# Performance work log

Measured on AMD Instinct MI355X. Metric: run time of the kernel, lower is better.

The kernel has to match this reference:

```python
import jax, jax.numpy as jnp
import numpy as np

N = 50000        # num nodes
E = 1_000_000    # num edges
F_IN = 256       # input feature dim
UNITS = 128      # hidden units
NUM_CLASSES = 40 # output classes
EPS = 1e-3       # Keras BatchNormalization default epsilon


def setup_inputs() -> dict:
    key = jax.random.key(0)
    ks = jax.random.split(key, 32)
    inp = {
        "x": jax.random.normal(ks[0], (N, F_IN), jnp.float32),
        "edge_index": jax.random.randint(ks[1], (2, E), 0, N, jnp.int32),
        "edge_weight": jax.random.uniform(ks[2], (E,), jnp.float32),
    }
    dims = [(F_IN, UNITS), (UNITS, UNITS), (UNITS, NUM_CLASSES)]
    ki = 3
    for li, (fi, fo) in enumerate(dims, 1):
        inp[f"w_gcn{li}"] = jax.random.normal(ks[ki], (fi, fo), jnp.float32) / np.sqrt(fi).astype(np.float32); ki += 1
        inp[f"w_self{li}"] = jax.random.normal(ks[ki], (fi, fo), jnp.float32) / np.sqrt(fi).astype(np.float32); ki += 1
        inp[f"b{li}"] = jnp.zeros((fo,), jnp.float32)
        inp[f"gamma{li}"] = 1.0 + 0.1 * jax.random.normal(ks[ki], (fo,), jnp.float32); ki += 1
        inp[f"beta{li}"] = 0.1 * jax.random.normal(ks[ki], (fo,), jnp.float32); ki += 1
        inp[f"mean{li}"] = 0.1 * jax.random.normal(ks[ki], (fo,), jnp.float32); ki += 1
        inp[f"var{li}"] = jnp.ones((fo,), jnp.float32)
    return inp


def _gcn_bs(h, src, dst, norm_w, w_gcn, w_self, b, gamma, beta, mean, var, act):
    # GCN aggregation: transform then gather->weight->scatter-sum
    hw = h @ w_gcn                                   # [N, out]
    msg = hw[src] * norm_w[:, None]                  # [E, out]
    agg = jax.ops.segment_sum(msg, dst, num_segments=N)
    out = agg + h @ w_self + b                       # self-loop dense + bias
    # BatchNorm (inference: moving stats)
    out = (out - mean) * jax.lax.rsqrt(var + EPS) * gamma + beta
    return act(out) if act is not None else out


def reference(x, edge_index, edge_weight,
              w_gcn1, w_self1, b1, gamma1, beta1, mean1, var1,
              w_gcn2, w_self2, b2, gamma2, beta2, mean2, var2,
              w_gcn3, w_self3, b3, gamma3, beta3, mean3, var3):
    src, dst = edge_index[0], edge_index[1]
    # symmetric GCN normalization (renorm=False: no added self loops)
    deg = jax.ops.segment_sum(edge_weight, dst, num_segments=N)
    dinv = jnp.where(deg > 0, jax.lax.rsqrt(jnp.where(deg > 0, deg, 1.0)), 0.0)
    norm_w = dinv[src] * edge_weight * dinv[dst]
    # inference: DropEdge and Dropout are identity
    h = _gcn_bs(x, src, dst, norm_w, w_gcn1, w_self1, b1, gamma1, beta1, mean1, var1, jax.nn.relu)
    h = _gcn_bs(h, src, dst, norm_w, w_gcn2, w_self2, b2, gamma2, beta2, mean2, var2, jax.nn.relu)
    h = _gcn_bs(h, src, dst, norm_w, w_gcn3, w_self3, b3, gamma3, beta3, mean3, var3, None)
    return h
```

## Files before the change

kernel.cpp:

```cpp
#include <hip/hip_runtime.h>
#include <hip/hip_bf16.h>

#define NN 50000
#define EE 1000000
static constexpr float EPSV = 1e-3f;
static constexpr float FIXSCALE = 16777216.f;

typedef __attribute__((ext_vector_type(8))) short short8;
typedef __attribute__((ext_vector_type(4))) float fx4;

__device__ inline float blo(unsigned u) { return __uint_as_float(u << 16); }
__device__ inline float bhi(unsigned u) { return __uint_as_float(u & 0xffff0000u); }
__device__ inline unsigned short f2b(float f) {
    __hip_bfloat16 h = __float2bfloat16(f);
    return *(unsigned short*)&h;
}
__device__ inline unsigned pack2(float a, float b) {
    return (unsigned)f2b(a) | ((unsigned)f2b(b) << 16);
}

__device__ inline void gload_lds16(const unsigned short* g, unsigned short* ldsbase) {
    __builtin_amdgcn_global_load_lds(
        (const __attribute__((address_space(1))) unsigned int*)(const void*)g,
        (__attribute__((address_space(3))) unsigned int*)(void*)ldsbase, 16, 0, 0);
}


#define ZB 391
#define WB1 256
#define WB2 128
#define WB3 64

__global__ void setup_kernel(float* __restrict__ zp,
                             const float* __restrict__ wg1, const float* __restrict__ ws1,
                             unsigned short* __restrict__ Wt1,
                             const float* __restrict__ wg2, const float* __restrict__ ws2,
                             unsigned short* __restrict__ Wt2,
                             const float* __restrict__ wg3, const float* __restrict__ ws3,
                             unsigned short* __restrict__ Wt3) {
    int b = blockIdx.x;
    int t = threadIdx.x;
    if (b < ZB) {
        int i = b * 256 + t;
        if (i < 100096) zp[i] = 0.f;
    } else if (b < ZB + WB1) {
        int idx = (b - ZB) * 256 + t;
        int n = idx >> 8, k = idx & 255;
        float v = (n < 128) ? wg1[(size_t)k * 128 + n]
                            : ws1[(size_t)k * 128 + (n - 128)];
        Wt1[idx] = f2b(v);
    } else if (b < ZB + WB1 + WB2) {
        int idx = (b - ZB - WB1) * 256 + t;
        int n = idx >> 7, k = idx & 127;
        float v = (n < 128) ? wg2[(size_t)k * 128 + n]
                            : ws2[(size_t)k * 128 + (n - 128)];
        Wt2[idx] = f2b(v);
    } else {
        int idx = (b - ZB - WB1 - WB2) * 256 + t;
        int n = idx >> 7, k = idx & 127;
        float v = 0.f;
        if (n < 40) v = wg3[(size_t)k * 40 + n];
        else if (n < 80) v = ws3[(size_t)k * 40 + (n - 40)];
        Wt3[idx] = f2b(v);
    }
}


template <bool AF32>
__device__ __forceinline__ void gemm_body(int bx, int by, const void* __restrict__ Av,
                                          const unsigned short* __restrict__ Wt,
                                          const float* __restrict__ bias,
                                          unsigned short* __restrict__ Cg,
                                          unsigned short* __restrict__ Cs,
                                          int M, int K, int Fo,
                                          unsigned short* sA, unsigned short* sB) {
    const int t = threadIdx.x;
    const int lane = t & 63;
    const int wave = t >> 6;
    const int wm = wave >> 1, wn = wave & 1;
    const int l15 = lane & 15, quad = lane >> 4;
    const int row0 = bx * 128;
    const int colbase = by * 128;

    fx4 acc[4][4];
#pragma unroll
    for (int r = 0; r < 4; ++r)
#pragma unroll
        for (int c = 0; c < 4; ++c) acc[r][c] = (fx4){0.f, 0.f, 0.f, 0.f};

    for (int kc = 0; kc < K; kc += 64) {
#pragma unroll
        for (int j = 0; j < 4; ++j) {
            int c = wave * 4 + j;
            int rb = c >> 1, kh = c & 1;
            int ar = row0 + rb * 16 + l15;
            if (ar >= M) ar = M - 1;
            int ak = kc + kh * 32 + quad * 8;
            if constexpr (AF32) {
                const float* Af = (const float*)Av;
                const float4* p = (const float4*)(Af + (size_t)ar * K + ak);
                float4 v0 = p[0], v1 = p[1];
                uint4 u;
                u.x = pack2(v0.x, v0.y);
                u.y = pack2(v0.z, v0.w);
                u.z = pack2(v1.x, v1.y);
                u.w = pack2(v1.z, v1.w);
                *reinterpret_cast<uint4*>(sA + c * 512 + lane * 8) = u;
            } else {
                gload_lds16((const unsigned short*)Av + (size_t)ar * K + ak, sA + c * 512);
            }
            int br = colbase + rb * 16 + l15;
            gload_lds16(Wt + (size_t)br * K + ak, sB + c * 512);
        }
        __syncthreads();

#pragma unroll
        for (int kh = 0; kh < 2; ++kh) {
            short8 a[4], b[4];
#pragma unroll
            for (int r = 0; r < 4; ++r)
                a[r] = *reinterpret_cast<const short8*>(&sA[((wm * 4 + r) * 2 + kh) * 512 + lane * 8]);
#pragma unroll
            for (int c = 0; c < 4; ++c)
                b[c] = *reinterpret_cast<const short8*>(&sB[((wn * 4 + c) * 2 + kh) * 512 + lane * 8]);
#pragma unroll
            for (int r = 0; r < 4; ++r)
#pragma unroll
                for (int c = 0; c < 4; ++c)
                    acc[r][c] = __builtin_amdgcn_mfma_f32_16x16x32_bf16(a[r], b[c], acc[r][c], 0, 0, 0);
        }
        __syncthreads();
    }

#pragma unroll
    for (int c = 0; c < 4; ++c) {
        int f = colbase + wn * 64 + c * 16 + l15;
        if (f >= 2 * Fo) continue;
        bool isG = (f < Fo);
        int col = isG ? f : f - Fo;
        float badd = isG ? 0.f : bias[col];
        unsigned short* base = isG ? Cg : Cs;
#pragma unroll
        for (int r = 0; r < 4; ++r) {
#pragma unroll
            for (int reg = 0; reg < 4; ++reg) {
                int row = row0 + wm * 64 + r * 16 + quad * 4 + reg;
                if (row < M) base[(size_t)row * Fo + col] = f2b(acc[r][c][reg] + badd);
            }
        }
    }
}


#define CB 3907
#define GX1 391

__global__ __launch_bounds__(256) void pre2_kernel(
    const int* __restrict__ ei, const float* __restrict__ ew,
    unsigned long long* __restrict__ cnt64, unsigned* __restrict__ rank,
    const float* __restrict__ x, const unsigned short* __restrict__ Wt1,
    const float* __restrict__ bias1,
    unsigned short* __restrict__ Cg, unsigned short* __restrict__ Cs) {
    __shared__ unsigned short sA[128 * 64];
    __shared__ unsigned short sB[128 * 64];
    int b = blockIdx.x;
    if (b < CB) {
        int e = b * 256 + threadIdx.x;
        if (e < EE) {
            int d = ei[EE + e];
            unsigned fx = __float2uint_rn(ew[e] * FIXSCALE);
            unsigned long long old =
                atomicAdd(&cnt64[d], 0x100000000ull | (unsigned long long)fx);
            rank[e] = (unsigned)(old >> 32);
        }
        return;
    }
    int gi = b - CB;
    int by = gi / GX1;
    int bx = gi - by * GX1;
    gemm_body<true>(bx, by, x, Wt1, bias1, Cg, Cs, NN, 256, 128, sA, sB);
}

template <bool AF32>
__global__ __launch_bounds__(256) void gemm_mfma(const void* __restrict__ Ab,
                                                 const unsigned short* __restrict__ Wt,
                                                 const float* __restrict__ bias,
                                                 unsigned short* __restrict__ Cg,
                                                 unsigned short* __restrict__ Cs,
                                                 int M, int K, int Fo) {
    __shared__ unsigned short sA[128 * 64];
    __shared__ unsigned short sB[128 * 64];
    gemm_body<AF32>(blockIdx.x, blockIdx.y, Ab, Wt, bias, Cg, Cs, M, K, Fo, sA, sB);
}


__global__ __launch_bounds__(1024) void dinvsum_kernel(const uint2* __restrict__ cnt64,
                                                       float* __restrict__ dinv,
                                                       int* __restrict__ bsum) {
    __shared__ int s[1024];
    const int t = threadIdx.x;
    int idx = blockIdx.x * 1024 + t;
    uint2 cv = make_uint2(0u, 0u);
    if (idx < NN) cv = cnt64[idx];
    float deg = (float)cv.x * (1.f / FIXSCALE);
    if (idx < NN) dinv[idx] = (deg > 0.f) ? rsqrtf(deg) : 0.f;
    s[t] = (int)cv.y;
    __syncthreads();
#pragma unroll
    for (int off = 512; off > 0; off >>= 1) {
        if (t < off) s[t] += s[t + off];
        __syncthreads();
    }
    if (t == 0) bsum[blockIdx.x] = s[0];
}

__global__ __launch_bounds__(64) void scanB_kernel(const int* __restrict__ bsum,
                                                   int* __restrict__ bpre, int nb) {
    int t = threadIdx.x;
    int v = (t < nb) ? bsum[t] : 0;
    int own = v;
#pragma unroll
    for (int off = 1; off < 64; off <<= 1) {
        int u = __shfl_up(v, off);
        if (t >= off) v += u;
    }
    if (t < nb) bpre[t] = v - own;
}

__global__ __launch_bounds__(1024) void scanC_kernel(const uint2* __restrict__ cnt64,
                                                     const int* __restrict__ bpre,
                                                     int* __restrict__ rowstart) {
    __shared__ int s[1024];
    const int t = threadIdx.x;
    int idx = blockIdx.x * 1024 + t;
    int v = (idx < NN) ? (int)cnt64[idx].y : 0;
    s[t] = v;
    __syncthreads();
#pragma unroll
    for (int off = 1; off < 1024; off <<= 1) {
        int u = (t >= off) ? s[t - off] : 0;
        __syncthreads();
        s[t] += u;
        __syncthreads();
    }
    if (idx < NN) rowstart[idx] = s[t] - v + bpre[blockIdx.x];
    if (idx == 0) rowstart[NN] = EE;
}

__global__ void fill_kernel(const int* __restrict__ ei, const float* __restrict__ ew,
                            const float* __restrict__ dinv, const int* __restrict__ rowstart,
                            const unsigned* __restrict__ rank, unsigned* __restrict__ eprec4) {
    int e = blockIdx.x * blockDim.x + threadIdx.x;
    if (e >= EE) return;
    int s = ei[e], d = ei[EE + e];
    int idx = rowstart[d] + (int)rank[e];
    float w = dinv[s] * ew[e] * dinv[d];
    eprec4[idx] = ((unsigned)s << 16) | (unsigned)f2b(w);
}


template <bool RELU>
__global__ __launch_bounds__(256) void agg128_kernel(
    const int* __restrict__ rowstart, const unsigned* __restrict__ eprec4,
    const unsigned* __restrict__ hw, const unsigned* __restrict__ selfC,
    const float* __restrict__ g, const float* __restrict__ be,
    const float* __restrict__ mu, const float* __restrict__ va,
    unsigned* __restrict__ out) {
    int wave = threadIdx.x >> 6;
    int lane = threadIdx.x & 63;
    int n = blockIdx.x * 4 + wave;
    if (n >= NN) return;
    unsigned scp = selfC[n * 64 + lane];
    float acc0 = blo(scp), acc1 = bhi(scp);
    int beg = rowstart[n], end = rowstart[n + 1];
    int i = beg;
    for (; i + 4 <= end; i += 4) {
        unsigned e0 = eprec4[i], e1 = eprec4[i + 1], e2 = eprec4[i + 2], e3 = eprec4[i + 3];
        unsigned v0 = hw[(e0 >> 16) * 64u + lane];
        unsigned v1 = hw[(e1 >> 16) * 64u + lane];
        unsigned v2 = hw[(e2 >> 16) * 64u + lane];
        unsigned v3 = hw[(e3 >> 16) * 64u + lane];
        float w0 = blo(e0), w1 = blo(e1), w2 = blo(e2), w3 = blo(e3);
        acc0 += blo(v0) * w0; acc1 += bhi(v0) * w0;
        acc0 += blo(v1) * w1; acc1 += bhi(v1) * w1;
        acc0 += blo(v2) * w2; acc1 += bhi(v2) * w2;
        acc0 += blo(v3) * w3; acc1 += bhi(v3) * w3;
    }
    for (; i < end; ++i) {
        unsigned e = eprec4[i];
        unsigned v = hw[(e >> 16) * 64u + lane];
        float w = blo(e);
        acc0 += blo(v) * w; acc1 += bhi(v) * w;
    }
    float2 m2 = reinterpret_cast<const float2*>(mu)[lane];
    float2 v2f = reinterpret_cast<const float2*>(va)[lane];
    float2 g2 = reinterpret_cast<const float2*>(g)[lane];
    float2 b2 = reinterpret_cast<const float2*>(be)[lane];
    float r0 = (acc0 - m2.x) * rsqrtf(v2f.x + EPSV) * g2.x + b2.x;
    float r1 = (acc1 - m2.y) * rsqrtf(v2f.y + EPSV) * g2.y + b2.y;
    if (RELU) {
        r0 = fmaxf(r0, 0.f);
        r1 = fmaxf(r1, 0.f);
    }
    out[n * 64 + lane] = pack2(r0, r1);
}


__global__ __launch_bounds__(256) void agg40_kernel(
    const int* __restrict__ rowstart, const unsigned* __restrict__ eprec4,
    const unsigned* __restrict__ hw, const unsigned* __restrict__ selfC,
    const float* __restrict__ g, const float* __restrict__ be,
    const float* __restrict__ mu, const float* __restrict__ va,
    float* __restrict__ out) {
    int wave = threadIdx.x >> 6;
    int lane = threadIdx.x & 63;
    int n = blockIdx.x * 4 + wave;
    if (n >= NN) return;
    int grp = lane / 20;
    int fl = lane - grp * 20;
    float acc0 = 0.f, acc1 = 0.f;
    int beg = rowstart[n], end = rowstart[n + 1];
    if (grp < 3) {
        for (int i = beg + grp; i < end; i += 3) {
            unsigned e = eprec4[i];
            unsigned v = hw[(e >> 16) * 20u + fl];
            float w = blo(e);
            acc0 += blo(v) * w;
            acc1 += bhi(v) * w;
        }
    }
    acc0 += __shfl(acc0, lane + 20) + __shfl(acc0, lane + 40);
    acc1 += __shfl(acc1, lane + 20) + __shfl(acc1, lane + 40);
    if (lane < 20) {
        int f0 = lane * 2;
        unsigned scp = selfC[n * 20 + lane];
        acc0 += blo(scp);
        acc1 += bhi(scp);
        float2 m2 = reinterpret_cast<const float2*>(mu)[lane];
        float2 v2f = reinterpret_cast<const float2*>(va)[lane];
        float2 g2 = reinterpret_cast<const float2*>(g)[lane];
        float2 b2 = reinterpret_cast<const float2*>(be)[lane];
        float r0 = (acc0 - m2.x) * rsqrtf(v2f.x + EPSV) * g2.x + b2.x;
        float r1 = (acc1 - m2.y) * rsqrtf(v2f.y + EPSV) * g2.y + b2.y;
        *reinterpret_cast<float2*>(&out[(size_t)n * 40 + f0]) = make_float2(r0, r1);
    }
}


extern "C" void kernel_launch(void* const* d_in, const int* in_sizes, int n_in,
                              void* d_out, int out_size, void* d_ws, size_t ws_size,
                              hipStream_t stream) {
    const float* x = (const float*)d_in[0];
    const int* ei = (const int*)d_in[1];
    const float* ew = (const float*)d_in[2];

    const float* wg[3]  = {(const float*)d_in[3],  (const float*)d_in[10], (const float*)d_in[17]};
    const float* wsf[3] = {(const float*)d_in[4],  (const float*)d_in[11], (const float*)d_in[18]};
    const float* bs[3]  = {(const float*)d_in[5],  (const float*)d_in[12], (const float*)d_in[19]};
    const float* gm[3]  = {(const float*)d_in[6],  (const float*)d_in[13], (const float*)d_in[20]};
    const float* bt[3]  = {(const float*)d_in[7],  (const float*)d_in[14], (const float*)d_in[21]};
    const float* mu[3]  = {(const float*)d_in[8],  (const float*)d_in[15], (const float*)d_in[22]};
    const float* vr[3]  = {(const float*)d_in[9],  (const float*)d_in[16], (const float*)d_in[23]};

    float* W = (float*)d_ws;
    unsigned long long* cnt64 = (unsigned long long*)W;
    float* dinv     = W + 100096;
    unsigned* rank  = (unsigned*)(W + 150144);
    int*   bsum     = (int*)(W + 1150144);
    int*   bpre     = (int*)(W + 1150208);
    int*   rowstart = (int*)(W + 1150272);
    unsigned* eprec4 = (unsigned*)(W + 1200384);
    unsigned short* Wt1 = (unsigned short*)(W + 2200384);
    unsigned short* Wt2 = (unsigned short*)(W + 2233152);
    unsigned short* Wt3 = (unsigned short*)(W + 2249536);
    unsigned short* bufH = (unsigned short*)(W + 2257728);
    unsigned short* bufHW = (unsigned short*)(W + 8657728);
    unsigned short* bufSb = (unsigned short*)(W + 11857728);

    const int B = 256;
    const int SB = 49;

    setup_kernel<<<ZB + WB1 + WB2 + WB3, B, 0, stream>>>(
        W, wg[0], wsf[0], Wt1, wg[1], wsf[1], Wt2, wg[2], wsf[2], Wt3);

    pre2_kernel<<<CB + 2 * GX1, B, 0, stream>>>(
        ei, ew, cnt64, rank, x, Wt1, bs[0], bufHW, bufSb);

    dinvsum_kernel<<<SB, 1024, 0, stream>>>((const uint2*)cnt64, dinv, bsum);
    scanB_kernel<<<1, 64, 0, stream>>>(bsum, bpre, SB);
    scanC_kernel<<<SB, 1024, 0, stream>>>((const uint2*)cnt64, bpre, rowstart);
    fill_kernel<<<(EE + B - 1) / B, B, 0, stream>>>(ei, ew, dinv, rowstart, rank, eprec4);

    const int aggGrid = (NN + 3) / 4;
    dim3 g2((NN + 127) / 128, 2), g1((NN + 127) / 128, 1);

    agg128_kernel<true><<<aggGrid, B, 0, stream>>>(rowstart, eprec4, (const unsigned*)bufHW,
                                                   (const unsigned*)bufSb, gm[0], bt[0], mu[0], vr[0],
                                                   (unsigned*)bufH);

    gemm_mfma<false><<<g2, B, 0, stream>>>(bufH, Wt2, bs[1], bufHW, bufSb, NN, 128, 128);
    agg128_kernel<true><<<aggGrid, B, 0, stream>>>(rowstart, eprec4, (const unsigned*)bufHW,
                                                   (const unsigned*)bufSb, gm[1], bt[1], mu[1], vr[1],
                                                   (unsigned*)bufH);

    gemm_mfma<false><<<g1, B, 0, stream>>>(bufH, Wt3, bs[2], bufHW, bufSb, NN, 128, 40);
    agg40_kernel<<<aggGrid, B, 0, stream>>>(rowstart, eprec4, (const unsigned*)bufHW,
                                            (const unsigned*)bufSb, gm[2], bt[2], mu[2], vr[2],
                                            (float*)d_out);
}
```

Before: 415.1 us.

## Specialize layer-1 GEMM with smaller tiles and batch degree-count atomics per thread

The fused pre-pass kernel gets a dedicated layer-1 GEMM that uses 64x128 tiles with a 32-wide K step and smaller LDS buffers, doubling the number of GEMM blocks. The degree-counting blocks now handle four edges per thread, issuing all loads before the atomics, so there are four times fewer counting blocks. The aim is better occupancy and load balance between the atomic work and the GEMM work in the shared launch, plus more memory-level parallelism in the counting phase. The trade-off is less A/B reuse per tile and more K-loop barriers in layer 1.

After: 424.1 us. +2.2%, slower.

```diff
diff --git a/kernel.cpp b/kernel.cpp
--- a/kernel.cpp
+++ b/kernel.cpp
@@ -66,21 +66,142 @@
 }
 
 
-template <bool AF32>
-__device__ __forceinline__ void gemm_body(int bx, int by, const void* __restrict__ Av,
-                                          const unsigned short* __restrict__ Wt,
-                                          const float* __restrict__ bias,
-                                          unsigned short* __restrict__ Cg,
-                                          unsigned short* __restrict__ Cs,
-                                          int M, int K, int Fo,
-                                          unsigned short* sA, unsigned short* sB) {
+#define CB4 977
+#define GX1 782
+#define GB1 1564
+
+__device__ __forceinline__ void gemm1_body(int bx, int by, const float* __restrict__ x,
+                                           const unsigned short* __restrict__ Wt,
+                                           const float* __restrict__ bias,
+                                           unsigned short* __restrict__ Cg,
+                                           unsigned short* __restrict__ Cs,
+                                           unsigned short* sA, unsigned short* sB) {
+    const int t = threadIdx.x;
+    const int lane = t & 63;
+    const int wave = t >> 6;
+    const int l15 = lane & 15, quad = lane >> 4;
+    const int row0 = bx * 64;
+    const int colbase = by * 128;
+
+    fx4 acc[4][2];
+#pragma unroll
+    for (int r = 0; r < 4; ++r)
+#pragma unroll
+        for (int c = 0; c < 2; ++c) acc[r][c] = (fx4){0.f, 0.f, 0.f, 0.f};
+
+    for (int kc = 0; kc < 256; kc += 32) {
+#pragma unroll
+        for (int j = 0; j < 3; ++j) {
+            int op = wave * 3 + j;
+            int ak = kc + quad * 8;
+            if (op < 4) {
+                int ar = row0 + op * 16 + l15;
+                if (ar >= NN) ar = NN - 1;
+                const float4* p = (const float4*)(x + (size_t)ar * 256 + ak);
+                float4 v0 = p[0], v1 = p[1];
+                uint4 u;
+                u.x = pack2(v0.x, v0.y);
+                u.y = pack2(v0.z, v0.w);
+                u.z = pack2(v1.x, v1.y);
+                u.w = pack2(v1.z, v1.w);
+                *reinterpret_cast<uint4*>(sA + op * 512 + lane * 8) = u;
+            } else {
+                int bi = op - 4;
+                int br = colbase + bi * 16 + l15;
+                gload_lds16(Wt + (size_t)br * 256 + ak, sB + bi * 512);
+            }
+        }
+        __syncthreads();
+
+        short8 a[4], bf[2];
+#pragma unroll
+        for (int r = 0; r < 4; ++r)
+            a[r] = *reinterpret_cast<const short8*>(&sA[r * 512 + lane * 8]);
+#pragma unroll
+        for (int c = 0; c < 2; ++c)
+            bf[c] = *reinterpret_cast<const short8*>(&sB[(wave * 2 + c) * 512 + lane * 8]);
+#pragma unroll
+        for (int r = 0; r < 4; ++r)
+#pragma unroll
+            for (int c = 0; c < 2; ++c)
+                acc[r][c] = __builtin_amdgcn_mfma_f32_16x16x32_bf16(a[r], bf[c], acc[r][c], 0, 0, 0);
+        __syncthreads();
+    }
+
+#pragma unroll
+    for (int c = 0; c < 2; ++c) {
+        int f = colbase + wave * 32 + c * 16 + l15;
+        bool isG = (f < 128);
+        int col = isG ? f : f - 128;
+        float badd = isG ? 0.f : bias[col];
+        unsigned short* basep = isG ? Cg : Cs;
+#pragma unroll
+        for (int r = 0; r < 4; ++r) {
+#pragma unroll
+            for (int reg = 0; reg < 4; ++reg) {
+                int row = row0 + r * 16 + quad * 4 + reg;
+                if (row < NN) basep[(size_t)row * 128 + col] = f2b(acc[r][c][reg] + badd);
+            }
+        }
+    }
+}
+
+__global__ __launch_bounds__(256) void pre2_kernel(
+    const int* __restrict__ ei, const float* __restrict__ ew,
+    unsigned long long* __restrict__ cnt64, unsigned* __restrict__ rank,
+    const float* __restrict__ x, const unsigned short* __restrict__ Wt1,
+    const float* __restrict__ bias1,
+    unsigned short* __restrict__ Cg, unsigned short* __restrict__ Cs) {
+    __shared__ unsigned short sA[64 * 32];
+    __shared__ unsigned short sB[128 * 32];
+    int b = blockIdx.x;
+    if (b < CB4) {
+        int base = b * 1024 + threadIdx.x;
+        int d[4];
+        unsigned fxv[4];
+        bool val[4];
+#pragma unroll
+        for (int k = 0; k < 4; ++k) {
+            int e = base + k * 256;
+            val[k] = (e < EE);
+            if (val[k]) {
+                d[k] = ei[EE + e];
+                fxv[k] = __float2uint_rn(ew[e] * FIXSCALE);
+            }
+        }
+#pragma unroll
+        for (int k = 0; k < 4; ++k) {
+            if (val[k]) {
+                unsigned long long old =
+                    atomicAdd(&cnt64[d[k]], 0x100000000ull | (unsigned long long)fxv[k]);
+                rank[base + k * 256] = (unsigned)(old >> 32);
+            }
+        }
+        return;
+    }
+    int gi = b - CB4;
+    int by = gi / GX1;
+    int bx = gi - by * GX1;
+    gemm1_body(bx, by, x, Wt1, bias1, Cg, Cs, sA, sB);
+}
+
+
+__global__ __launch_bounds__(256) void gemm_mfma(const unsigned short* __restrict__ Ab,
+                                                 const unsigned short* __restrict__ Wt,
+                                                 const float* __restrict__ bias,
+                                                 unsigned short* __restrict__ Cg,
+                                                 unsigned short* __restrict__ Cs,
+                                                 int M, int K, int Fo) {
+    __shared__ unsigned short sA[128 * 64];
+    __shared__ unsigned short sB[128 * 64];
+
     const int t = threadIdx.x;
     const int lane = t & 63;
     const int wave = t >> 6;
     const int wm = wave >> 1, wn = wave & 1;
     const int l15 = lane & 15, quad = lane >> 4;
-    const int row0 = bx * 128;
-    const int colbase = by * 128;
+    const int row0 = blockIdx.x * 128;
+    const int colbase = blockIdx.y * 128;
 
     fx4 acc[4][4];
 #pragma unroll
@@ -96,19 +217,7 @@
             int ar = row0 + rb * 16 + l15;
             if (ar >= M) ar = M - 1;
             int ak = kc + kh * 32 + quad * 8;
-            if constexpr (AF32) {
-                const float* Af = (const float*)Av;
-                const float4* p = (const float4*)(Af + (size_t)ar * K + ak);
-                float4 v0 = p[0], v1 = p[1];
-                uint4 u;
-                u.x = pack2(v0.x, v0.y);
-                u.y = pack2(v0.z, v0.w);
-                u.z = pack2(v1.x, v1.y);
-                u.w = pack2(v1.z, v1.w);
-                *reinterpret_cast<uint4*>(sA + c * 512 + lane * 8) = u;
-            } else {
-                gload_lds16((const unsigned short*)Av + (size_t)ar * K + ak, sA + c * 512);
-            }
+            gload_lds16(Ab + (size_t)ar * K + ak, sA + c * 512);
             int br = colbase + rb * 16 + l15;
             gload_lds16(Wt + (size_t)br * K + ak, sB + c * 512);
         }
@@ -149,48 +258,6 @@
             }
         }
     }
-}
-
-
-#define CB 3907
-#define GX1 391
-
-__global__ __launch_bounds__(256) void pre2_kernel(
-    const int* __restrict__ ei, const float* __restrict__ ew,
-    unsigned long long* __restrict__ cnt64, unsigned* __restrict__ rank,
-    const float* __restrict__ x, const unsigned short* __restrict__ Wt1,
-    const float* __restrict__ bias1,
-    unsigned short* __restrict__ Cg, unsigned short* __restrict__ Cs) {
-    __shared__ unsigned short sA[128 * 64];
-    __shared__ unsigned short sB[128 * 64];
-    int b = blockIdx.x;
-    if (b < CB) {
-        int e = b * 256 + threadIdx.x;
-        if (e < EE) {
-            int d = ei[EE + e];
-            unsigned fx = __float2uint_rn(ew[e] * FIXSCALE);
-            unsigned long long old =
-                atomicAdd(&cnt64[d], 0x100000000ull | (unsigned long long)fx);
-            rank[e] = (unsigned)(old >> 32);
-        }
-        return;
-    }
-    int gi = b - CB;
-    int by = gi / GX1;
-    int bx = gi - by * GX1;
-    gemm_body<true>(bx, by, x, Wt1, bias1, Cg, Cs, NN, 256, 128, sA, sB);
-}
-
-template <bool AF32>
-__global__ __launch_bounds__(256) void gemm_mfma(const void* __restrict__ Ab,
-                                                 const unsigned short* __restrict__ Wt,
-                                                 const float* __restrict__ bias,
-                                                 unsigned short* __restrict__ Cg,
-                                                 unsigned short* __restrict__ Cs,
-                                                 int M, int K, int Fo) {
-    __shared__ unsigned short sA[128 * 64];
-    __shared__ unsigned short sB[128 * 64];
-    gemm_body<AF32>(blockIdx.x, blockIdx.y, Ab, Wt, bias, Cg, Cs, M, K, Fo, sA, sB);
 }
 
 
@@ -383,7 +450,7 @@
     setup_kernel<<<ZB + WB1 + WB2 + WB3, B, 0, stream>>>(
         W, wg[0], wsf[0], Wt1, wg[1], wsf[1], Wt2, wg[2], wsf[2], Wt3);
 
-    pre2_kernel<<<CB + 2 * GX1, B, 0, stream>>>(
+    pre2_kernel<<<CB4 + GB1, B, 0, stream>>>(
         ei, ew, cnt64, rank, x, Wt1, bs[0], bufHW, bufSb);
 
     dinvsum_kernel<<<SB, 1024, 0, stream>>>((const uint2*)cnt64, dinv, bsum);
@@ -398,12 +465,12 @@
                                                    (const unsigned*)bufSb, gm[0], bt[0], mu[0], vr[0],
                                                    (unsigned*)bufH);
 
-    gemm_mfma<false><<<g2, B, 0, stream>>>(bufH, Wt2, bs[1], bufHW, bufSb, NN, 128, 128);
+    gemm_mfma<<<g2, B, 0, stream>>>(bufH, Wt2, bs[1], bufHW, bufSb, NN, 128, 128);
     agg128_kernel<true><<<aggGrid, B, 0, stream>>>(rowstart, eprec4, (const unsigned*)bufHW,
                                                    (const unsigned*)bufSb, gm[1], bt[1], mu[1], vr[1],
                                                    (unsigned*)bufH);
 
-    gemm_mfma<false><<<g1, B, 0, stream>>>(bufH, Wt3, bs[2], bufHW, bufSb, NN, 128, 40);
+    gemm_mfma<<<g1, B, 0, stream>>>(bufH, Wt3, bs[2], bufHW, bufSb, NN, 128, 40);
     agg40_kernel<<<aggGrid, B, 0, stream>>>(rowstart, eprec4, (const unsigned*)bufHW,
                                             (const unsigned*)bufSb, gm[2], bt[2], mu[2], vr[2],
                                             (float*)d_out);
```
